# Optimization experiments

Measured on AMD Instinct MI355X. Metric: run time of the kernel, lower is better.

Reference implementation:

```python
import jax, jax.numpy as jnp
import numpy as np

BS = 256          # batch_size
NN = BS - 1
D = 128           # projection dim
SIGMA = 0.07      # rbf gamma (self.sigma)
C = 1.0
REG = 0.1
NUM_ITERS = 1000
ETA = 0.001
USE_NORM = True


def setup_inputs() -> dict:
    key = jax.random.key(0)
    k1, k2 = jax.random.split(key)
    z = jax.random.normal(k1, (BS, 2, D), dtype=jnp.float32)
    alpha_init = jax.random.normal(k2, (BS, NN, 1), dtype=jnp.float32)
    return {"z": z, "alpha_init": alpha_init}


def _rbf_kernel(X, Y, gamma):
    # exp(-gamma * ||x - y||^2)
    xn = jnp.sum(X * X, axis=1, keepdims=True)          # [n,1]
    yn = jnp.sum(Y * Y, axis=1, keepdims=True).T        # [1,m]
    d = xn + yn - 2.0 * (X @ Y.T)
    return jnp.exp(-gamma * d)


def _pgd_nesterov(DD, p, alpha0, eta, num_iters, C, use_norm):
    # minimize 0.5 a'DDa - p'a  s.t. 0 <= a <= C, batched over bs
    def step(carry, t):
        alpha, alpha_prev = carry
        beta = t / (t + 3.0)
        y = alpha + beta * (alpha - alpha_prev)
        grad = jnp.einsum('bij,bjk->bik', DD, y) - p     # [bs,nn,1]
        if use_norm:
            grad = grad / (jnp.linalg.norm(grad, axis=1, keepdims=True) + 1e-12)
        alpha_new = jnp.clip(y - eta * grad, 0.0, C)
        return (alpha_new, alpha), None
    (alpha, _), _ = jax.lax.scan(step, (alpha0, alpha0),
                                 jnp.arange(num_iters, dtype=jnp.float32))
    return alpha


def reference(z, alpha_init):
    bs, nn = BS, NN
    # F.normalize(z, p=2, dim=1): normalize over the view axis (faithful to source)
    nrm = jnp.maximum(jnp.linalg.norm(z, axis=1, keepdims=True), 1e-12)
    ftr = z / nrm
    ftr = jnp.concatenate([ftr[:, 0, :], ftr[:, 1, :]], axis=0)   # [2bs, d]

    K = _rbf_kernel(ftr[:bs], ftr, SIGMA)                          # [bs, 2bs]

    # ---- QP construction + solve under no_grad ----
    Kd = jax.lax.stop_gradient(K)
    KK = Kd[:, :bs]                                                # block: first bs cols
    r = jnp.arange(bs)
    m = jnp.arange(nn)
    # idx[i] = [0..bs-1] without i  (KMASK row/col removal)
    idx = m[None, :] + (m[None, :] >= r[:, None]).astype(jnp.int32)  # [bs, nn]
    KK_sub = KK[idx[:, :, None], idx[:, None, :]]                  # [bs,nn,nn]
    row = jnp.take_along_axis(KK, idx, axis=1)                     # row[i,m]=KK[i,idx[i,m]]
    # Delta[i,j,k] = 1 + reg*d_jk + KK[j,k] - KK[i,j] - KK[i,k]  (j,k != i)
    DD = (1.0 + REG * jnp.eye(nn, dtype=KK.dtype)[None]
          + KK_sub - row[:, :, None] - row[:, None, :])            # [bs,nn,nn]

    p = 2.0 * jnp.ones((bs, nn, 1), dtype=jnp.float32)
    alpha0 = jnp.clip(jax.nn.relu(alpha_init), 0.0, C)
    alpha = _pgd_nesterov(DD, p, alpha0, ETA, NUM_ITERS, C, USE_NORM)
    alpha_y = jnp.clip(jax.nn.relu(alpha[:, :, 0]), 0.0, C)
    alpha_y = jax.lax.stop_gradient(alpha_y)                       # [bs,nn]
    alpha_x = alpha_y.sum(axis=1)                                  # [bs]

    # ---- loss terms (grad flows through K here) ----
    Ks = K[:, bs:]                                                 # block12: [bs,bs]
    # Kn.T[i,m] = Ks.T[i, idx[i,m]]  (neg_mask = off-diagonal)
    KnT = jnp.take_along_axis(Ks.T, idx, axis=1)                   # [bs,nn]
    pos = jnp.diagonal(Ks)                                         # pos_mask = eye
    pos_loss = jnp.mean(alpha_x * pos)
    neg_loss = jnp.sum(alpha_y * KnT) / bs
    loss = neg_loss - pos_loss

    sparsity = ((alpha_y == C).sum().astype(jnp.float32)
                / ((alpha_y > 0).sum().astype(jnp.float32) + 1e-10))
    num_zero = (alpha_y == 0.0).mean()
    return (loss, pos.mean(), KnT.mean(), sparsity, num_zero, jnp.float32(0.0))
```

## Files before the change

### kernel.cpp

```cpp
#include <hip/hip_runtime.h>
#include <math.h>

#define BS   256
#define NN   255
#define DIM  128
#define GAMMA 0.07
#define NUM_ITERS 1000

typedef float v2f __attribute__((ext_vector_type(2)));

__device__ __forceinline__ double wred_d(double v) {
  #pragma unroll
  for (int k = 1; k < 64; k <<= 1) v += __shfl_xor(v, k, 64);
  return v;
}
__device__ __forceinline__ int wred_i(int v) {
  #pragma unroll
  for (int k = 1; k < 64; k <<= 1) v += __shfl_xor(v, k, 64);
  return v;
}

__device__ __forceinline__ float RLF(float v, int lane) {
  return __int_as_float(__builtin_amdgcn_readlane(__float_as_int(v), lane));
}

template <int CTRL, int RMASK>
__device__ __forceinline__ float dpp_add(float x) {
  int t = __builtin_amdgcn_update_dpp(0, __float_as_int(x), CTRL, RMASK, 0xf, true);
  return x + __int_as_float(t);
}
__device__ __forceinline__ float wred64_dpp(float x) {
  x = dpp_add<0x111, 0xf>(x);
  x = dpp_add<0x112, 0xf>(x);
  x = dpp_add<0x114, 0xf>(x);
  x = dpp_add<0x118, 0xf>(x);
  x = dpp_add<0x142, 0xa>(x);
  x = dpp_add<0x143, 0xc>(x);
  return RLF(x, 63);
}

__device__ __forceinline__ float bfly8(float x) {
  int t = __builtin_amdgcn_update_dpp(0, __float_as_int(x), 0x128, 0xf, 0xf, true);
  return x + __int_as_float(t);
}
__device__ __forceinline__ float bfly16(float x) {
#if __has_builtin(__builtin_amdgcn_permlane16_swap)
  unsigned u = __float_as_uint(x);
  auto p = __builtin_amdgcn_permlane16_swap(u, u, false, false);
  return __uint_as_float(p[0]) + __uint_as_float(p[1]);
#else
  return x + __shfl_xor(x, 16, 64);
#endif
}
__device__ __forceinline__ float bfly32(float x) {
#if __has_builtin(__builtin_amdgcn_permlane32_swap)
  unsigned u = __float_as_uint(x);
  auto p = __builtin_amdgcn_permlane32_swap(u, u, false, false);
  return __uint_as_float(p[0]) + __uint_as_float(p[1]);
#else
  return x + __shfl_xor(x, 32, 64);
#endif
}

__device__ __forceinline__ float rsq_nr(float x) {
  float r;
  asm("v_rsq_f32 %0, %1" : "=v"(r) : "v"(x));
  r = r * (1.5f - 0.5f * x * r * r);
  return r;
}

__device__ __forceinline__ void pk_fma(v2f& acc, const v2f& k, const v2f& y) {
  asm("v_pk_fma_f32 %0, %1, %2, %0" : "+v"(acc) : "v"(k), "v"(y));
}

__global__ void k_ftr(const float* __restrict__ z, double* __restrict__ ftrT) {
  int b = blockIdx.x;
  int d = threadIdx.x;
  double z0 = (double)z[b * 256 + d];
  double z1 = (double)z[b * 256 + 128 + d];
  double n = sqrt(z0 * z0 + z1 * z1);
  n = fmax(n, 1e-12);
  ftrT[d * 512 + b]       = z0 / n;
  ftrT[d * 512 + 256 + b] = z1 / n;
}

__global__ void k_K(const double* __restrict__ ftrT, float* __restrict__ K,
                    double* __restrict__ pk_knt, double* __restrict__ pos_arr) {
  int i = blockIdx.x;
  int t = threadIdx.x;
  __shared__ double rowi[DIM];
  __shared__ double redd[4];
  if (t < DIM) rowi[t] = ftrT[t * 512 + i];
  __syncthreads();
  double xn = 0.0;
  #pragma unroll 8
  for (int d = 0; d < DIM; ++d) xn += rowi[d] * rowi[d];

  double knt_part = 0.0;
  #pragma unroll
  for (int h = 0; h < 2; ++h) {
    int j = t + h * 256;
    double dot = 0.0, sq = 0.0;
    #pragma unroll 8
    for (int d = 0; d < DIM; ++d) {
      double f = ftrT[d * 512 + j];
      dot += rowi[d] * f;
      sq  += f * f;
    }
    double dist = xn + sq - 2.0 * dot;
    double kv = exp(-GAMMA * dist);
    K[i * 512 + j] = (float)kv;
    if (h == 1) {
      if (j == 256 + i) pos_arr[i] = kv;
      else knt_part += kv;
    }
  }
  double w = wred_d(knt_part);
  if ((t & 63) == 0) redd[t >> 6] = w;
  __syncthreads();
  if (t == 0) pk_knt[i] = redd[0] + redd[1] + redd[2] + redd[3];
}

__global__ __launch_bounds__(512, 2) void k_pgd(
    const float* __restrict__ K, const float* __restrict__ alpha_init,
    double* __restrict__ neg_arr, double* __restrict__ sa_arr,
    int* __restrict__ cnt1, int* __restrict__ cntp, int* __restrict__ cnt0) {
  int r = blockIdx.x;
  int tid = threadIdx.x;
  int l = tid & 63;
  int rg = tid >> 6;
  int m = l >> 3;
  int cb = 32 * rg + 4 * (l & 7);

  __shared__ __align__(16) float ytil2[8 * 36];
  __shared__ __align__(16) float gAshare[2][BS];
  __shared__ float betat[1024];

  for (int i = tid; i < 1024; i += 512)
    betat[i] = (float)i / ((float)i + 3.0f);

  v2f kq[64];
  #pragma unroll
  for (int j = 0; j < 16; ++j) {
    float4 r0 = *(const float4*)&K[(32 * m + 2 * j + 0) * 512 + cb];
    float4 r1 = *(const float4*)&K[(32 * m + 2 * j + 1) * 512 + cb];
    kq[j].x      = r0.x; kq[j].y      = r1.x;
    kq[16 + j].x = r0.y; kq[16 + j].y = r1.y;
    kq[32 + j].x = r0.z; kq[32 + j].y = r1.z;
    kq[48 + j].x = r0.w; kq[48 + j].y = r1.w;
  }
  #pragma unroll
  for (int j = 0; j < 64; ++j)
    asm volatile("" : "+v"(kq[j]));

  float al[4], ap[4], yv[4], kv[4], rm2[4];
  #pragma unroll
  for (int k = 0; k < 4; ++k) {
    int a = 4 * l + k;
    if (a == r) {
      al[k] = 0.f; ap[k] = 0.f; yv[k] = 0.f; kv[k] = 0.f; rm2[k] = 0.f;
    } else {
      int c = a - (a > r ? 1 : 0);
      float v = alpha_init[r * NN + c];
      v = fminf(fmaxf(v, 0.f), 1.f);
      al[k] = v; ap[k] = v; yv[k] = v;
      kv[k] = 1.0f - K[r * 512 + a];
      rm2[k] = 2.0f;
    }
  }
  {
    float4 y4 = {yv[0], yv[1], yv[2], yv[3]};
    *(float4*)&ytil2[36 * (l >> 3) + ((4 * l) & 31)] = y4;
  }
  __syncthreads();

  int rq = r >> 2, rc = r & 3;

  for (int it = 0; it < NUM_ITERS; ++it) {
    float beta = betat[it + 1];

    const float4* yb = (const float4*)&ytil2[36 * m];
    v2f a0 = {0.f, 0.f}, a1 = {0.f, 0.f}, a2 = {0.f, 0.f}, a3 = {0.f, 0.f};
    #pragma unroll
    for (int jj = 0; jj < 8; ++jj) {
      float4 yq = yb[jj];
      v2f ylo = {yq.x, yq.y};
      v2f yhi = {yq.z, yq.w};
      pk_fma(a0, kq[2 * jj],      ylo); pk_fma(a0, kq[2 * jj + 1],      yhi);
      pk_fma(a1, kq[16 + 2 * jj], ylo); pk_fma(a1, kq[16 + 2 * jj + 1], yhi);
      pk_fma(a2, kq[32 + 2 * jj], ylo); pk_fma(a2, kq[32 + 2 * jj + 1], yhi);
      pk_fma(a3, kq[48 + 2 * jj], ylo); pk_fma(a3, kq[48 + 2 * jj + 1], yhi);
    }
    float4 accw = {a0.x + a0.y, a1.x + a1.y, a2.x + a2.y, a3.x + a3.y};
    accw.x = bfly8(accw.x);  accw.y = bfly8(accw.y);
    accw.z = bfly8(accw.z);  accw.w = bfly8(accw.w);
    accw.x = bfly16(accw.x); accw.y = bfly16(accw.y);
    accw.z = bfly16(accw.z); accw.w = bfly16(accw.w);
    accw.x = bfly32(accw.x); accw.y = bfly32(accw.y);
    accw.z = bfly32(accw.z); accw.w = bfly32(accw.w);
    if (l < 8) *(float4*)&gAshare[it & 1][32 * rg + 4 * l] = accw;

    float Sv = wred64_dpp((yv[0] + yv[1]) + (yv[2] + yv[3]));
    __syncthreads();

    float4 gA = *(const float4*)&gAshare[it & 1][4 * l];
    float grv = (rc == 0) ? gA.x : (rc == 1) ? gA.y : (rc == 2) ? gA.z : gA.w;
    float gr = RLF(grv, rq);
    float g[4];
    g[0] = (gA.x - gr) - rm2[0] + kv[0] * Sv + 0.1f * yv[0];
    g[1] = (gA.y - gr) - rm2[1] + kv[1] * Sv + 0.1f * yv[1];
    g[2] = (gA.z - gr) - rm2[2] + kv[2] * Sv + 0.1f * yv[2];
    g[3] = (gA.w - gr) - rm2[3] + kv[3] * Sv + 0.1f * yv[3];
    float n2 = wred64_dpp((g[0] * g[0] + g[1] * g[1]) + (g[2] * g[2] + g[3] * g[3]));
    float sinv = 0.001f * rsq_nr(n2);
    #pragma unroll
    for (int k = 0; k < 4; ++k) {
      float na = fminf(fmaxf(fmaf(-sinv, g[k], yv[k]), 0.f), 1.f);
      ap[k] = al[k];
      al[k] = na;
      yv[k] = fmaf(beta, na - ap[k], na);
    }
    float4 y4 = {yv[0], yv[1], yv[2], yv[3]};
    *(float4*)&ytil2[36 * (l >> 3) + ((4 * l) & 31)] = y4;
  }

  if (rg == 0) {
    double nl = 0.0, sa = 0.0;
    int c1 = 0, cp = 0, cz = 0;
    #pragma unroll
    for (int k = 0; k < 4; ++k) {
      int a = 4 * l + k;
      if (a != r) {
        float kx = K[a * 512 + 256 + r];
        nl += (double)al[k] * (double)kx;
        sa += (double)al[k];
        c1 += (al[k] == 1.0f);
        cp += (al[k] > 0.0f);
        cz += (al[k] == 0.0f);
      }
    }
    nl = wred_d(nl); sa = wred_d(sa);
    c1 = wred_i(c1); cp = wred_i(cp); cz = wred_i(cz);
    if (l == 0) {
      neg_arr[r] = nl;
      sa_arr[r]  = sa;
      cnt1[r] = c1; cntp[r] = cp; cnt0[r] = cz;
    }
  }
}

__global__ void k_fin(const double* __restrict__ pk_knt, const double* __restrict__ pos_arr,
                      const double* __restrict__ neg_arr, const double* __restrict__ sa_arr,
                      const int* __restrict__ cnt1, const int* __restrict__ cntp,
                      const int* __restrict__ cnt0, float* __restrict__ out) {
  int t = threadIdx.x;
  __shared__ double rd[16];
  __shared__ int ri[12];
  double knt = pk_knt[t];
  double pos = pos_arr[t];
  double neg = neg_arr[t];
  double pl  = sa_arr[t] * pos_arr[t];
  int a1 = cnt1[t], ap = cntp[t], a0 = cnt0[t];
  knt = wred_d(knt); pos = wred_d(pos); neg = wred_d(neg); pl = wred_d(pl);
  a1 = wred_i(a1); ap = wred_i(ap); a0 = wred_i(a0);
  int w = t >> 6;
  if ((t & 63) == 0) {
    rd[w] = knt; rd[4 + w] = pos; rd[8 + w] = neg; rd[12 + w] = pl;
    ri[w] = a1; ri[4 + w] = ap; ri[8 + w] = a0;
  }
  __syncthreads();
  if (t == 0) {
    double kntS = rd[0] + rd[1] + rd[2] + rd[3];
    double posS = rd[4] + rd[5] + rd[6] + rd[7];
    double negS = rd[8] + rd[9] + rd[10] + rd[11];
    double plS  = rd[12] + rd[13] + rd[14] + rd[15];
    int c1t = ri[0] + ri[1] + ri[2] + ri[3];
    int cpt = ri[4] + ri[5] + ri[6] + ri[7];
    int c0t = ri[8] + ri[9] + ri[10] + ri[11];
    out[0] = (float)(negS / 256.0 - plS / 256.0);
    out[1] = (float)(posS / 256.0);
    out[2] = (float)(kntS / (256.0 * 255.0));
    out[3] = (float)c1t / ((float)cpt + 1e-10f);
    out[4] = (float)c0t / 65280.0f;
    out[5] = 0.0f;
  }
}

extern "C" void kernel_launch(void* const* d_in, const int* in_sizes, int n_in,
                              void* d_out, int out_size, void* d_ws, size_t ws_size,
                              hipStream_t stream) {
  const float* z     = (const float*)d_in[0];
  const float* ainit = (const float*)d_in[1];
  char* ws = (char*)d_ws;
  double* ftrT   = (double*)ws;
  float*  K      = (float*)(ws + 524288);
  double* pk_knt = (double*)(ws + 1048576);
  double* pos_a  = (double*)(ws + 1048576 + 2048);
  double* neg_a  = (double*)(ws + 1048576 + 4096);
  double* sa_a   = (double*)(ws + 1048576 + 6144);
  int* cnt1 = (int*)(ws + 1048576 + 8192);
  int* cntp = (int*)(ws + 1048576 + 8192 + 1024);
  int* cnt0 = (int*)(ws + 1048576 + 8192 + 2048);
  float* out = (float*)d_out;

  k_ftr<<<256, 128, 0, stream>>>(z, ftrT);
  k_K  <<<256, 256, 0, stream>>>(ftrT, K, pk_knt, pos_a);
  k_pgd<<<256, 512, 0, stream>>>(K, ainit, neg_a, sa_a, cnt1, cntp, cnt0);
  k_fin<<<1, 256, 0, stream>>>(pk_knt, pos_a, neg_a, sa_a, cnt1, cntp, cnt0, out);
}
```

Measured before the change: 913.8 us.

## Repartition PGD matvec so each wave owns a row block, reduce via LDS

Changes the per-block work split of the PGD matvec. Each wave now holds a 32-row stripe of K across all 256 columns, instead of each lane group holding column slices. Partial sums go to an LDS partial array and are reduced across waves after the barrier. Norm and sum reductions become intra-8-lane DPP plus a second barrier through LDS. This trades the full 64-lane cross-wave shuffles and replicated y-state for an extra __syncthreads per iteration and more LDS traffic.

```diff
diff --git a/kernel.cpp b/kernel.cpp
--- a/kernel.cpp
+++ b/kernel.cpp
@@ -20,23 +20,10 @@
   return v;
 }
 
-__device__ __forceinline__ float RLF(float v, int lane) {
-  return __int_as_float(__builtin_amdgcn_readlane(__float_as_int(v), lane));
-}
-
 template <int CTRL, int RMASK>
 __device__ __forceinline__ float dpp_add(float x) {
   int t = __builtin_amdgcn_update_dpp(0, __float_as_int(x), CTRL, RMASK, 0xf, true);
   return x + __int_as_float(t);
-}
-__device__ __forceinline__ float wred64_dpp(float x) {
-  x = dpp_add<0x111, 0xf>(x);
-  x = dpp_add<0x112, 0xf>(x);
-  x = dpp_add<0x114, 0xf>(x);
-  x = dpp_add<0x118, 0xf>(x);
-  x = dpp_add<0x142, 0xa>(x);
-  x = dpp_add<0x143, 0xc>(x);
-  return RLF(x, 63);
 }
 
 __device__ __forceinline__ float bfly8(float x) {
@@ -129,12 +116,14 @@
   int tid = threadIdx.x;
   int l = tid & 63;
   int rg = tid >> 6;
-  int m = l >> 3;
-  int cb = 32 * rg + 4 * (l & 7);
-
-  __shared__ __align__(16) float ytil2[8 * 36];
-  __shared__ __align__(16) float gAshare[2][BS];
+
+  __shared__ __align__(16) float part[8][264];
+  __shared__ __align__(16) float ytil[BS];
   __shared__ float betat[1024];
+  __shared__ float P_lds[8];
+  __shared__ float Sy_lds[8];
+  __shared__ double dred[2][8];
+  __shared__ int ired[3][8];
 
   for (int i = tid; i < 1024; i += 512)
     betat[i] = (float)i / ((float)i + 3.0f);
@@ -142,8 +131,8 @@
   v2f kq[64];
   #pragma unroll
   for (int j = 0; j < 16; ++j) {
-    float4 r0 = *(const float4*)&K[(32 * m + 2 * j + 0) * 512 + cb];
-    float4 r1 = *(const float4*)&K[(32 * m + 2 * j + 1) * 512 + cb];
+    float4 r0 = *(const float4*)&K[(32 * rg + 2 * j + 0) * 512 + 4 * l];
+    float4 r1 = *(const float4*)&K[(32 * rg + 2 * j + 1) * 512 + 4 * l];
     kq[j].x      = r0.x; kq[j].y      = r1.x;
     kq[16 + j].x = r0.y; kq[16 + j].y = r1.y;
     kq[32 + j].x = r0.z; kq[32 + j].y = r1.z;
@@ -153,10 +142,11 @@
   for (int j = 0; j < 64; ++j)
     asm volatile("" : "+v"(kq[j]));
 
+  int c0 = 32 * rg + 4 * (l & 7);
   float al[4], ap[4], yv[4], kv[4], rm2[4];
   #pragma unroll
   for (int k = 0; k < 4; ++k) {
-    int a = 4 * l + k;
+    int a = c0 + k;
     if (a == r) {
       al[k] = 0.f; ap[k] = 0.f; yv[k] = 0.f; kv[k] = 0.f; rm2[k] = 0.f;
     } else {
@@ -168,18 +158,22 @@
       rm2[k] = 2.0f;
     }
   }
+  if ((l >> 3) == 0) {
+    float4 y4 = {yv[0], yv[1], yv[2], yv[3]};
+    *(float4*)&ytil[32 * rg + 4 * l] = y4;
+  }
   {
-    float4 y4 = {yv[0], yv[1], yv[2], yv[3]};
-    *(float4*)&ytil2[36 * (l >> 3) + ((4 * l) & 31)] = y4;
+    float sy = (yv[0] + yv[1]) + (yv[2] + yv[3]);
+    sy = dpp_add<0x111, 0xf>(sy);
+    sy = dpp_add<0x112, 0xf>(sy);
+    sy = dpp_add<0x114, 0xf>(sy);
+    if (l == 7) Sy_lds[rg] = sy;
   }
   __syncthreads();
 
-  int rq = r >> 2, rc = r & 3;
-
+  float g[4];
   for (int it = 0; it < NUM_ITERS; ++it) {
-    float beta = betat[it + 1];
-
-    const float4* yb = (const float4*)&ytil2[36 * m];
+    const float4* yb = (const float4*)&ytil[32 * rg];
     v2f a0 = {0.f, 0.f}, a1 = {0.f, 0.f}, a2 = {0.f, 0.f}, a3 = {0.f, 0.f};
     #pragma unroll
     for (int jj = 0; jj < 8; ++jj) {
@@ -192,27 +186,33 @@
       pk_fma(a3, kq[48 + 2 * jj], ylo); pk_fma(a3, kq[48 + 2 * jj + 1], yhi);
     }
     float4 accw = {a0.x + a0.y, a1.x + a1.y, a2.x + a2.y, a3.x + a3.y};
-    accw.x = bfly8(accw.x);  accw.y = bfly8(accw.y);
-    accw.z = bfly8(accw.z);  accw.w = bfly8(accw.w);
-    accw.x = bfly16(accw.x); accw.y = bfly16(accw.y);
-    accw.z = bfly16(accw.z); accw.w = bfly16(accw.w);
-    accw.x = bfly32(accw.x); accw.y = bfly32(accw.y);
-    accw.z = bfly32(accw.z); accw.w = bfly32(accw.w);
-    if (l < 8) *(float4*)&gAshare[it & 1][32 * rg + 4 * l] = accw;
-
-    float Sv = wred64_dpp((yv[0] + yv[1]) + (yv[2] + yv[3]));
+    *(float4*)&part[rg][4 * l] = accw;
     __syncthreads();
 
-    float4 gA = *(const float4*)&gAshare[it & 1][4 * l];
-    float grv = (rc == 0) ? gA.x : (rc == 1) ? gA.y : (rc == 2) ? gA.z : gA.w;
-    float gr = RLF(grv, rq);
-    float g[4];
+    float Sv = ((Sy_lds[7] + Sy_lds[6]) + (Sy_lds[5] + Sy_lds[4]))
+             + ((Sy_lds[3] + Sy_lds[2]) + (Sy_lds[1] + Sy_lds[0]));
+    float p0 = part[0][r], p1 = part[1][r], p2 = part[2][r], p3 = part[3][r];
+    float p4 = part[4][r], p5 = part[5][r], p6 = part[6][r], p7 = part[7][r];
+    float gr = ((p0 + p1) + (p2 + p3)) + ((p4 + p5) + (p6 + p7));
+    float4 gA = *(const float4*)&part[l >> 3][32 * rg + 4 * (l & 7)];
+    gA.x = bfly8(gA.x);  gA.y = bfly8(gA.y);  gA.z = bfly8(gA.z);  gA.w = bfly8(gA.w);
+    gA.x = bfly16(gA.x); gA.y = bfly16(gA.y); gA.z = bfly16(gA.z); gA.w = bfly16(gA.w);
+    gA.x = bfly32(gA.x); gA.y = bfly32(gA.y); gA.z = bfly32(gA.z); gA.w = bfly32(gA.w);
     g[0] = (gA.x - gr) - rm2[0] + kv[0] * Sv + 0.1f * yv[0];
     g[1] = (gA.y - gr) - rm2[1] + kv[1] * Sv + 0.1f * yv[1];
     g[2] = (gA.z - gr) - rm2[2] + kv[2] * Sv + 0.1f * yv[2];
     g[3] = (gA.w - gr) - rm2[3] + kv[3] * Sv + 0.1f * yv[3];
-    float n2 = wred64_dpp((g[0] * g[0] + g[1] * g[1]) + (g[2] * g[2] + g[3] * g[3]));
+    float s = (g[0] * g[0] + g[1] * g[1]) + (g[2] * g[2] + g[3] * g[3]);
+    s = dpp_add<0x111, 0xf>(s);
+    s = dpp_add<0x112, 0xf>(s);
+    s = dpp_add<0x114, 0xf>(s);
+    if (l == 7) P_lds[rg] = s;
+    __syncthreads();
+
+    float n2 = ((P_lds[7] + P_lds[6]) + (P_lds[5] + P_lds[4]))
+             + ((P_lds[3] + P_lds[2]) + (P_lds[1] + P_lds[0]));
     float sinv = 0.001f * rsq_nr(n2);
+    float beta = betat[it + 1];
     #pragma unroll
     for (int k = 0; k < 4; ++k) {
       float na = fminf(fmaxf(fmaf(-sinv, g[k], yv[k]), 0.f), 1.f);
@@ -220,16 +220,23 @@
       al[k] = na;
       yv[k] = fmaf(beta, na - ap[k], na);
     }
-    float4 y4 = {yv[0], yv[1], yv[2], yv[3]};
-    *(float4*)&ytil2[36 * (l >> 3) + ((4 * l) & 31)] = y4;
-  }
-
-  if (rg == 0) {
+    if ((l >> 3) == 0) {
+      float4 y4 = {yv[0], yv[1], yv[2], yv[3]};
+      *(float4*)&ytil[32 * rg + 4 * l] = y4;
+    }
+    float sy = (yv[0] + yv[1]) + (yv[2] + yv[3]);
+    sy = dpp_add<0x111, 0xf>(sy);
+    sy = dpp_add<0x112, 0xf>(sy);
+    sy = dpp_add<0x114, 0xf>(sy);
+    if (l == 7) Sy_lds[rg] = sy;
+  }
+
+  {
     double nl = 0.0, sa = 0.0;
     int c1 = 0, cp = 0, cz = 0;
     #pragma unroll
     for (int k = 0; k < 4; ++k) {
-      int a = 4 * l + k;
+      int a = c0 + k;
       if (a != r) {
         float kx = K[a * 512 + 256 + r];
         nl += (double)al[k] * (double)kx;
@@ -239,12 +246,33 @@
         cz += (al[k] == 0.0f);
       }
     }
-    nl = wred_d(nl); sa = wred_d(sa);
-    c1 = wred_i(c1); cp = wred_i(cp); cz = wred_i(cz);
+    #pragma unroll
+    for (int k = 1; k <= 4; k <<= 1) {
+      nl += __shfl_xor(nl, k, 64);
+      sa += __shfl_xor(sa, k, 64);
+      c1 += __shfl_xor(c1, k, 64);
+      cp += __shfl_xor(cp, k, 64);
+      cz += __shfl_xor(cz, k, 64);
+    }
     if (l == 0) {
-      neg_arr[r] = nl;
-      sa_arr[r]  = sa;
-      cnt1[r] = c1; cntp[r] = cp; cnt0[r] = cz;
+      dred[0][rg] = nl; dred[1][rg] = sa;
+      ired[0][rg] = c1; ired[1][rg] = cp; ired[2][rg] = cz;
+    }
+    __syncthreads();
+    if (tid == 0) {
+      double nlT = ((dred[0][0] + dred[0][1]) + (dred[0][2] + dred[0][3]))
+                 + ((dred[0][4] + dred[0][5]) + (dred[0][6] + dred[0][7]));
+      double saT = ((dred[1][0] + dred[1][1]) + (dred[1][2] + dred[1][3]))
+                 + ((dred[1][4] + dred[1][5]) + (dred[1][6] + dred[1][7]));
+      int c1T = ired[0][0] + ired[0][1] + ired[0][2] + ired[0][3]
+              + ired[0][4] + ired[0][5] + ired[0][6] + ired[0][7];
+      int cpT = ired[1][0] + ired[1][1] + ired[1][2] + ired[1][3]
+              + ired[1][4] + ired[1][5] + ired[1][6] + ired[1][7];
+      int czT = ired[2][0] + ired[2][1] + ired[2][2] + ired[2][3]
+              + ired[2][4] + ired[2][5] + ired[2][6] + ired[2][7];
+      neg_arr[r] = nlT;
+      sa_arr[r]  = saT;
+      cnt1[r] = c1T; cntp[r] = cpT; cnt0[r] = czT;
     }
   }
 }
```

Result: slower. 1.070 ms (+17.0%).
